# Optimization experiments

Measured on AMD Instinct MI355X. Metric: run time of the kernel, lower is better.

## Reference

```python
import jax, jax.numpy as jnp
import numpy as np
import math

# Config (matches init_kwargs): ProphetNet-style ngram self-attention
T, B, E, H, NGRAM, NB, MAXD = 512, 4, 1024, 16, 2, 32, 128
HD = E // H
TGT = (1 + NGRAM) * T
NEG = -1e9


def _buckets(rel):
    # faithful numpy version of _relative_positions_bucket (bidirectional=False)
    n = np.maximum(-rel, 0)
    max_exact = NB // 2
    is_small = n < max_exact
    large = max_exact + np.log(np.maximum(n, 1) / max_exact) / math.log(MAXD / max_exact) * (NB - max_exact)
    large = np.minimum(large, NB - 1).astype(np.int32)
    return np.where(is_small, n.astype(np.int32), large)


def setup_inputs() -> dict:
    key = jax.random.key(0)
    ks = jax.random.split(key, 4)
    s = 0.02
    # position ids 1..T (ProphetNet positions start at 1); precompute bucket tables
    pos = np.arange(1, T + 1, dtype=np.int64)[None, :].repeat(B, axis=0)          # [B,T]
    main_rel = pos[:, None, :] - pos[:, :, None]                                  # [B,T,T]
    pred_keys = np.concatenate([pos - 1, pos], axis=-1)                           # [B,2T]
    pred_rel = pred_keys[:, None, :] - pos[:, :, None]                            # [B,T,2T]
    return {
        "query": jax.random.normal(ks[0], (TGT, B, E), jnp.float32),
        "in_proj_weight": jax.random.normal(ks[1], (3 * E, E), jnp.float32) * s,
        "in_proj_bias": jnp.zeros((3 * E,), jnp.float32),
        "rel_w": jax.random.normal(ks[2], (NB * H, E), jnp.float32) * s,
        "rel_b": jnp.zeros((NB * H,), jnp.float32),
        "out_w": jax.random.normal(ks[3], (E, E), jnp.float32) * s,
        "out_b": jnp.zeros((E,), jnp.float32),
        "main_buckets": jnp.asarray(_buckets(main_rel), jnp.int32),
        "predict_buckets": jnp.asarray(_buckets(pred_rel), jnp.int32),
    }


def reference(query, in_proj_weight, in_proj_bias, rel_w, rel_b, out_w, out_b,
              main_buckets, predict_buckets):
    scaling = HD ** -0.5
    qkv = query @ in_proj_weight.T + in_proj_bias                  # [TGT,B,3E]
    q, k, v = jnp.split(qkv, 3, axis=-1)
    q = q * scaling

    def heads(x):  # [TGT,B,E] -> [B*H, TGT, HD]
        return x.reshape(TGT, B * H, HD).transpose(1, 0, 2)

    q, k, v = heads(q), heads(k), heads(v)
    q_main, k_main, v_main = q[:, :T], k[:, :T], v[:, :T]

    def ngram_split(x):  # [B*H, NGRAM*T, HD] -> [N, B*H, T, HD]
        return x[:, T:].reshape(B * H, NGRAM, T, HD).transpose(1, 0, 2, 3)

    q_pred, k_pred, v_pred = ngram_split(q), ngram_split(k), ngram_split(v)
    h_main = query[:T]                                             # [T,B,E]
    h_pred = query[T:].reshape(NGRAM, T, B, E)

    # ---------- main stream ----------
    aw_main = jnp.einsum('bth,bsh->bts', q_main, k_main)           # [B*H,T,T]
    vals = h_main.transpose(1, 0, 2) @ rel_w.T + rel_b             # [B,T,NB*H]
    vals = vals.reshape(B, T, NB, H).transpose(0, 3, 1, 2)         # [B,H,T,NB]
    idx = jnp.broadcast_to(main_buckets[:, None], (B, H, T, T))
    rel_main = jnp.take_along_axis(vals, idx, axis=-1).reshape(B * H, T, T)
    causal = jnp.triu(jnp.full((T, T), NEG, jnp.float32), 1)       # self_attn_mask
    aw_main = jax.nn.softmax(aw_main + rel_main + causal[None], axis=-1)
    attn_main = jnp.einsum('bts,bsh->bth', aw_main, v_main)        # [B*H,T,HD]
    attn_main = attn_main.transpose(1, 0, 2).reshape(1, T, B, E)
    attn_main = attn_main @ out_w.T + out_b

    # ---------- ngram predict streams ----------
    k_ng = jnp.concatenate([jnp.broadcast_to(k_main[None], (NGRAM, B * H, T, HD)), k_pred], axis=2)
    v_ng = jnp.concatenate([jnp.broadcast_to(v_main[None], (NGRAM, B * H, T, HD)), v_pred], axis=2)
    aw_ng = jnp.einsum('nbtc,nbsc->nbts', q_pred, k_ng)            # [N,B*H,T,2T]
    valsn = h_pred.transpose(0, 2, 1, 3) @ rel_w.T + rel_b         # [N,B,T,NB*H]
    valsn = valsn.reshape(NGRAM, B, T, NB, H).transpose(0, 1, 4, 2, 3)  # [N,B,H,T,NB]
    idxn = jnp.broadcast_to(predict_buckets[None, :, None], (NGRAM, B, H, T, 2 * T))
    rel_ng = jnp.take_along_axis(valsn, idxn, axis=-1).reshape(NGRAM, B * H, T, 2 * T)
    # ngram_mask: main part causal, predict part only the matching position
    ng_mask = jnp.concatenate([causal, NEG * (1.0 - jnp.eye(T, dtype=jnp.float32))], axis=1)  # [T,2T]
    aw_ng = jax.nn.softmax(aw_ng + rel_ng + ng_mask[None, None], axis=-1)
    attn_ng = jnp.einsum('nbts,nbsc->nbtc', aw_ng, v_ng)           # [N,B*H,T,HD]
    attn_ng = attn_ng.transpose(0, 2, 1, 3).reshape(NGRAM, T, B, E)
    attn_ng = attn_ng @ out_w.T + out_b

    return jnp.concatenate([attn_main, attn_ng], axis=0).reshape(TGT, B, E)
```

## Files before the change

kernel.cpp:

```cpp
#include <hip/hip_runtime.h>
#include <hip/hip_bf16.h>
#include <math.h>

constexpr int T_ = 512;
constexpr int B_ = 4;
constexpr int E_ = 1024;
constexpr int H_ = 16;
constexpr int NGRAM_ = 2;
constexpr int TGT_ = (1 + NGRAM_) * T_;
constexpr int ROWS_ = TGT_ * B_;

typedef __bf16 bf16_t;
typedef __bf16 bf16x8 __attribute__((ext_vector_type(8)));
typedef __bf16 bf16x4 __attribute__((ext_vector_type(4)));
typedef float f32x4 __attribute__((ext_vector_type(4)));

#define GLL(gaddr, laddr)                                                     \
  __builtin_amdgcn_global_load_lds(                                           \
      (const __attribute__((address_space(1))) void*)(gaddr),                 \
      (__attribute__((address_space(3))) void*)(laddr), 16, 0, 0)

#define BARX()  asm volatile("s_barrier" ::: "memory")
#define WVM7()  asm volatile("s_waitcnt vmcnt(7)" ::: "memory")
#define WVM0()  asm volatile("s_waitcnt vmcnt(0)" ::: "memory")
#define LGKM0() asm volatile("s_waitcnt lgkmcnt(0)" ::: "memory")

__global__ __launch_bounds__(256) void prep(
    const float* __restrict__ query, const float* __restrict__ ipw,
    const float* __restrict__ relw, const float* __restrict__ outw,
    bf16_t* __restrict__ qb, bf16_t* __restrict__ ipwb,
    bf16_t* __restrict__ relwb, bf16_t* __restrict__ outwb) {
  const int i = blockIdx.x * 256 + threadIdx.x;
  constexpr int N1 = ROWS_ * E_ / 4;
  constexpr int N2 = 3 * E_ * E_ / 4;
  constexpr int N3 = 512 * E_ / 4;
  constexpr int N4 = E_ * E_ / 4;
  const float4* src;
  bf16_t* dst;
  int j = i;
  if (i < N1) { src = (const float4*)query; dst = qb; }
  else if (i < N1 + N2) { src = (const float4*)ipw; dst = ipwb; j = i - N1; }
  else if (i < N1 + N2 + N3) { src = (const float4*)relw; dst = relwb; j = i - N1 - N2; }
  else if (i < N1 + N2 + N3 + N4) { src = (const float4*)outw; dst = outwb; j = i - N1 - N2 - N3; }
  else return;
  const float4 v = src[j];
  bf16x4 o;
  o[0] = (bf16_t)v.x; o[1] = (bf16_t)v.y;
  o[2] = (bf16_t)v.z; o[3] = (bf16_t)v.w;
  ((bf16x4*)dst)[j] = o;
}

__device__ __forceinline__ int sw256(int row, int col) {
  return row * 256 + ((((col >> 3) ^ (row & 31)) << 3) | (col & 7));
}

__global__ __launch_bounds__(512, 2) void bgemm_proj(
    const bf16_t* __restrict__ A, const bf16_t* __restrict__ W,
    const float* __restrict__ ipb, const float* __restrict__ relb,
    bf16_t* __restrict__ qkvb, float* __restrict__ relv2,
    bf16_t* __restrict__ vT) {
  __shared__ bf16_t smem[57344];
  bf16_t* As0 = smem;
  bf16_t* As1 = smem + 12288;
  bf16_t* Bs0 = smem + 24576;
  bf16_t* Bs1 = smem + 24576 + 16384;

  const int tid = threadIdx.x;
  const int wave = tid >> 6, lane = tid & 63;
  const int wr = wave >> 2, wc = wave & 3;
  const int pid = blockIdx.y * 14 + blockIdx.x;
  const int lid = (pid & 7) * 56 + (pid >> 3);
  const int by = lid / 14;
  const int bx = lid - by * 14;
  const int bm = by * 192, bn = bx * 256;
  const int q = lane >> 4, ln = lane & 15;
  const int grow = tid >> 3;
  const int gcol = ((tid & 7) ^ (grow & 7)) * 8;
  const int co[2] = {((q) ^ (ln & 7)) * 8, ((4 + q) ^ (ln & 7)) * 8};

  f32x4 acc[6][4];
#pragma unroll
  for (int mi = 0; mi < 6; ++mi)
#pragma unroll
    for (int ni = 0; ni < 4; ++ni)
#pragma unroll
      for (int r = 0; r < 4; ++r) acc[mi][ni][r] = 0.f;

  auto stage = [&](int kt, bf16_t* la, bf16_t* lb) {
    const int kc = kt * 64 + gcol;
#pragma unroll
    for (int p = 0; p < 3; ++p)
      GLL(&A[(size_t)(bm + p * 64 + grow) * 1024 + kc], &la[p * 4096 + tid * 8]);
#pragma unroll
    for (int p = 0; p < 4; ++p)
      GLL(&W[(size_t)(bn + p * 64 + grow) * 1024 + kc], &lb[p * 4096 + tid * 8]);
  };

  auto compute = [&](const bf16_t* la, const bf16_t* lb) {
#pragma unroll
    for (int t = 0; t < 2; ++t) {
      bf16x8 bfr[4], afr[3];
#pragma unroll
      for (int ni = 0; ni < 4; ++ni)
        bfr[ni] = *(const bf16x8*)&lb[(wc * 64 + ni * 16 + ln) * 64 + co[t]];
#pragma unroll
      for (int mi = 0; mi < 3; ++mi)
        afr[mi] = *(const bf16x8*)&la[(wr * 96 + mi * 16 + ln) * 64 + co[t]];
      BARX(); LGKM0();
      __builtin_amdgcn_s_setprio(1);
#pragma unroll
      for (int mi = 0; mi < 3; ++mi)
#pragma unroll
        for (int ni = 0; ni < 4; ++ni)
          acc[mi][ni] = __builtin_amdgcn_mfma_f32_16x16x32_bf16(
              afr[mi], bfr[ni], acc[mi][ni], 0, 0, 0);
      __builtin_amdgcn_s_setprio(0);
      BARX();
#pragma unroll
      for (int mi = 0; mi < 3; ++mi)
        afr[mi] = *(const bf16x8*)&la[(wr * 96 + (3 + mi) * 16 + ln) * 64 + co[t]];
      BARX(); LGKM0();
      __builtin_amdgcn_s_setprio(1);
#pragma unroll
      for (int mi = 0; mi < 3; ++mi)
#pragma unroll
        for (int ni = 0; ni < 4; ++ni)
          acc[3 + mi][ni] = __builtin_amdgcn_mfma_f32_16x16x32_bf16(
              afr[mi], bfr[ni], acc[3 + mi][ni], 0, 0, 0);
      __builtin_amdgcn_s_setprio(0);
      BARX();
    }
  };

  stage(0, As0, Bs0);
  stage(1, As1, Bs1);

  for (int jj = 0; jj < 8; ++jj) {
    WVM7(); BARX();
    compute(As0, Bs0);
    if (jj < 7) stage(2 * jj + 2, As0, Bs0);
    if (jj < 7) { WVM7(); } else { WVM0(); }
    BARX();
    compute(As1, Bs1);
    if (jj < 7) stage(2 * jj + 3, As1, Bs1);
  }

  if (bn < 2048) {
    const float sc = (bn < 1024) ? 0.125f : 1.0f;
#pragma unroll
    for (int mi = 0; mi < 6; ++mi) {
#pragma unroll
      for (int ni = 0; ni < 4; ++ni) {
        const int col = bn + wc * 64 + ni * 16 + ln;
        const float bv = ipb[col];
#pragma unroll
        for (int r = 0; r < 4; ++r) {
          const int row = bm + wr * 96 + mi * 16 + q * 4 + r;
          qkvb[(size_t)row * 3072 + col] = (bf16_t)((acc[mi][ni][r] + bv) * sc);
        }
      }
    }
  } else if (bn < 3072) {
    __syncthreads();
#pragma unroll
    for (int mi = 0; mi < 6; ++mi) {
#pragma unroll
      for (int ni = 0; ni < 4; ++ni) {
        const int col_l = wc * 64 + ni * 16 + ln;
        const float bv = ipb[bn + col_l];
#pragma unroll
        for (int r = 0; r < 4; ++r) {
          const int row_l = wr * 96 + mi * 16 + q * 4 + r;
          smem[sw256(row_l, col_l)] = (bf16_t)(acc[mi][ni][r] + bv);
        }
      }
    }
    __syncthreads();
    const int h0 = (bn - 2048) >> 6;
    const int tb0 = bm >> 2;
#pragma unroll
    for (int e = 0; e < 2; ++e) {
      const int task = e * 512 + tid;
      const int b = task & 3;
      const int c = task >> 2;
      const int h = h0 + (c >> 6);
      const int d = c & 63;
      const size_t base = ((size_t)((b * 16 + h) * 64 + d)) * (size_t)TGT_ + tb0;
#pragma unroll
      for (int k = 0; k < 6; ++k) {
        bf16x8 v8;
#pragma unroll
        for (int i = 0; i < 8; ++i)
          v8[i] = smem[sw256((k * 8 + i) * 4 + b, c)];
        *(bf16x8*)&vT[base + k * 8] = v8;
      }
    }
  } else {
    const int cb = bn - 3072 + wc * 64;
    float4 rb4;
#pragma unroll
    for (int ni = 0; ni < 4; ++ni)
      ((float*)&rb4)[ni] = relb[cb + ni * 16 + ln];
    const int bkbase = cb >> 4;
#pragma unroll
    for (int mi = 0; mi < 6; ++mi) {
#pragma unroll
      for (int r = 0; r < 4; ++r) {
        const int row = bm + wr * 96 + mi * 16 + q * 4 + r;
        float4 v;
        v.x = acc[mi][0][r] + rb4.x;
        v.y = acc[mi][1][r] + rb4.y;
        v.z = acc[mi][2][r] + rb4.z;
        v.w = acc[mi][3][r] + rb4.w;
        *(float4*)&relv2[(size_t)row * 512 + ln * 32 + bkbase] = v;
      }
    }
  }
}

__global__ __launch_bounds__(256, 4) void bgemm_out(
    const bf16_t* __restrict__ A, const bf16_t* __restrict__ W,
    const float* __restrict__ bias, float* __restrict__ C, int N) {
  __shared__ bf16_t As[128 * 64];
  __shared__ bf16_t Bs[128 * 64];

  const int tid = threadIdx.x;
  const int wave = tid >> 6, lane = tid & 63;
  const int wr = wave >> 1, wc = wave & 1;
  const int pid = blockIdx.y * 8 + blockIdx.x;
  const int lid = (pid & 7) * 48 + (pid >> 3);
  const int bm = (lid >> 3) * 128, bn = (lid & 7) * 128;
  const int q = lane >> 4, ln = lane & 15;
  const int grow = tid >> 3;
  const int gcol = ((tid & 7) ^ (grow & 7)) * 8;

  f32x4 acc[4][4];
#pragma unroll
  for (int mi = 0; mi < 4; ++mi)
#pragma unroll
    for (int ni = 0; ni < 4; ++ni)
#pragma unroll
      for (int r = 0; r < 4; ++r) acc[mi][ni][r] = 0.f;

  const int co[2] = {((q) ^ (ln & 7)) * 8, ((4 + q) ^ (ln & 7)) * 8};

  for (int k0 = 0; k0 < 1024; k0 += 64) {
    __syncthreads();
#pragma unroll
    for (int p = 0; p < 4; ++p) {
      GLL(&A[(size_t)(bm + p * 32 + grow) * 1024 + k0 + gcol], &As[p * 2048 + tid * 8]);
      GLL(&W[(size_t)(bn + p * 32 + grow) * 1024 + k0 + gcol], &Bs[p * 2048 + tid * 8]);
    }
    __syncthreads();
#pragma unroll
    for (int t = 0; t < 2; ++t) {
      bf16x8 af[4], bf[4];
#pragma unroll
      for (int mi = 0; mi < 4; ++mi)
        af[mi] = *(const bf16x8*)&As[(wr * 64 + mi * 16 + ln) * 64 + co[t]];
#pragma unroll
      for (int ni = 0; ni < 4; ++ni)
        bf[ni] = *(const bf16x8*)&Bs[(wc * 64 + ni * 16 + ln) * 64 + co[t]];
#pragma unroll
      for (int mi = 0; mi < 4; ++mi)
#pragma unroll
        for (int ni = 0; ni < 4; ++ni)
          acc[mi][ni] = __builtin_amdgcn_mfma_f32_16x16x32_bf16(
              af[mi], bf[ni], acc[mi][ni], 0, 0, 0);
    }
  }

#pragma unroll
  for (int mi = 0; mi < 4; ++mi) {
#pragma unroll
    for (int ni = 0; ni < 4; ++ni) {
      const int col = bn + wc * 64 + ni * 16 + ln;
      const float bv = bias[col];
#pragma unroll
      for (int r = 0; r < 4; ++r) {
        const int row = bm + wr * 64 + mi * 16 + q * 4 + r;
        C[(size_t)row * N + col] = acc[mi][ni][r] + bv;
      }
    }
  }
}

__device__ __forceinline__ int bucket_of(int n) {
  if (n < 16) return n;
  const float lf = __log2f((float)n);
  int b = (int)(16.0f + (lf - 4.0f) * 5.3333333f);
  return b > 31 ? 31 : b;
}

__global__ __launch_bounds__(256, 2) void flash_mfma(
    const bf16_t* __restrict__ qkvb, const bf16_t* __restrict__ vT,
    const float* __restrict__ relv2, bf16_t* __restrict__ attn) {
  __shared__ bf16_t Ks[2][64 * 64];
  __shared__ bf16_t Vts[2][64 * 64];
  __shared__ bf16_t Ps[4][16 * 64];
  __shared__ bf16_t biasS[3][64 * 33];

  const int qt = 7 - blockIdx.x, tq0 = qt * 64;
  const int bh = blockIdx.y, b = bh >> 4, h = bh & 15;
  const int tid = threadIdx.x;
  const int wave = tid >> 6, lane = tid & 63;
  const int q = lane >> 4, ln = lane & 15;
  const int m0 = wave * 16;
  const int grow = tid >> 3;
  const int gcol = ((tid & 7) ^ (grow & 7)) * 8;
  const int co[2] = {((q) ^ (ln & 7)) * 8, ((4 + q) ^ (ln & 7)) * 8};

#pragma unroll
  for (int z = 0; z < 3; ++z) {
#pragma unroll
    for (int u = 0; u < 2; ++u) {
      const int c = u * 256 + tid;
      const int row = c >> 3, j4 = (c & 7) * 4;
      const float4 v = *(const float4*)
          &relv2[((size_t)(z * T_ + tq0 + row) * B_ + b) * 512 + h * 32 + j4];
      biasS[z][row * 33 + j4 + 0] = (bf16_t)v.x;
      biasS[z][row * 33 + j4 + 1] = (bf16_t)v.y;
      biasS[z][row * 33 + j4 + 2] = (bf16_t)v.z;
      biasS[z][row * 33 + j4 + 3] = (bf16_t)v.w;
    }
  }

#pragma unroll
  for (int u = 0; u < 2; ++u) {
    const int sr = u * 32 + grow;
    GLL(&qkvb[((size_t)(0 * T_ + tq0 + sr) * B_ + b) * 3072 + h * 64 + gcol],
        &Ks[0][u * 2048 + tid * 8]);
    GLL(&qkvb[((size_t)(1 * T_ + tq0 + sr) * B_ + b) * 3072 + h * 64 + gcol],
        &Vts[0][u * 2048 + tid * 8]);
    GLL(&qkvb[((size_t)(2 * T_ + tq0 + sr) * B_ + b) * 3072 + h * 64 + gcol],
        &Ks[1][u * 2048 + tid * 8]);
  }
  __syncthreads();

  bf16x8 aq[3][2];
  aq[0][0] = *(const bf16x8*)&Ks[0][(m0 + ln) * 64 + co[0]];
  aq[0][1] = *(const bf16x8*)&Ks[0][(m0 + ln) * 64 + co[1]];
  aq[1][0] = *(const bf16x8*)&Vts[0][(m0 + ln) * 64 + co[0]];
  aq[1][1] = *(const bf16x8*)&Vts[0][(m0 + ln) * 64 + co[1]];
  aq[2][0] = *(const bf16x8*)&Ks[1][(m0 + ln) * 64 + co[0]];
  aq[2][1] = *(const bf16x8*)&Ks[1][(m0 + ln) * 64 + co[1]];

  float bv31[3][4], bv0[3][4];
#pragma unroll
  for (int z = 0; z < 3; ++z)
#pragma unroll
    for (int r = 0; r < 4; ++r) {
      const int rloc = m0 + q * 4 + r;
      bv31[z][r] = (float)biasS[z][rloc * 33 + 31];
      bv0[z][r] = (float)biasS[z][rloc * 33];
    }

  f32x4 Od[3][4];
  float lpart[3][4];
#pragma unroll
  for (int z = 0; z < 3; ++z)
#pragma unroll
    for (int r = 0; r < 4; ++r) {
      lpart[z][r] = 0.f;
#pragma unroll
      for (int tc = 0; tc < 4; ++tc) Od[z][tc][r] = 0.f;
    }

  const int ntiles = qt + 3;

  auto stage_tile = [&](int jj, int buf) {
    const int krb = (jj <= qt) ? jj * 64 : ((jj - qt) * T_ + tq0);
#pragma unroll
    for (int u = 0; u < 2; ++u) {
      const int sr = u * 32 + grow;
      GLL(&qkvb[((size_t)(krb + sr) * B_ + b) * 3072 + 1024 + h * 64 + gcol],
          &Ks[buf][u * 2048 + tid * 8]);
      GLL(&vT[((size_t)bh * 64 + sr) * (size_t)TGT_ + krb + gcol],
          &Vts[buf][u * 2048 + tid * 8]);
    }
  };

  __syncthreads();
  stage_tile(0, 0);
  __syncthreads();

  for (int jj = 0; jj < ntiles; ++jj) {
    const int cur = jj & 1;
    if (jj + 1 < ntiles) stage_tile(jj + 1, cur ^ 1);

    const int krb = (jj <= qt) ? jj * 64 : ((jj - qt) * T_ + tq0);

    bf16x8 kf[4][2], vf[4][2];
#pragma unroll
    for (int tc = 0; tc < 4; ++tc) {
      kf[tc][0] = *(const bf16x8*)&Ks[cur][(tc * 16 + ln) * 64 + co[0]];
      kf[tc][1] = *(const bf16x8*)&Ks[cur][(tc * 16 + ln) * 64 + co[1]];
      vf[tc][0] = *(const bf16x8*)&Vts[cur][(tc * 16 + ln) * 64 + co[0]];
      vf[tc][1] = *(const bf16x8*)&Vts[cur][(tc * 16 + ln) * 64 + co[1]];
    }

    if (jj <= qt) {
      const bool far = (jj <= qt - 3);
#pragma unroll
      for (int z = 0; z < 3; ++z) {
        f32x4 acc[4];
#pragma unroll
        for (int tc = 0; tc < 4; ++tc)
#pragma unroll
          for (int r = 0; r < 4; ++r) acc[tc][r] = 0.f;
#pragma unroll
        for (int tc = 0; tc < 4; ++tc) {
          acc[tc] = __builtin_amdgcn_mfma_f32_16x16x32_bf16(aq[z][0], kf[tc][0], acc[tc], 0, 0, 0);
          acc[tc] = __builtin_amdgcn_mfma_f32_16x16x32_bf16(aq[z][1], kf[tc][1], acc[tc], 0, 0, 0);
        }

        if (far) {
#pragma unroll
          for (int r = 0; r < 4; ++r) {
            const float bv = bv31[z][r];
#pragma unroll
            for (int tc = 0; tc < 4; ++tc) {
              const float p = __expf(acc[tc][r] + bv);
              lpart[z][r] += p;
              const int pc = (tc * 2 + (ln >> 3)) ^ ((q * 4 + r) & 7);
              Ps[wave][(q * 4 + r) * 64 + pc * 8 + (ln & 7)] = (bf16_t)p;
            }
          }
        } else {
#pragma unroll
          for (int r = 0; r < 4; ++r) {
            const int rloc = m0 + q * 4 + r;
            const int dbase = tq0 + rloc - krb;
#pragma unroll
            for (int tc = 0; tc < 4; ++tc) {
              const int sl = tc * 16 + ln;
              const int d = dbase - sl;
              const bool valid = (jj < qt) | (d >= 0);
              int n = d < 0 ? 0 : d;
              if (z > 0) n += 1;
              const float bv = (float)biasS[z][rloc * 33 + bucket_of(n)];
              const float p = valid ? __expf(acc[tc][r] + bv) : 0.f;
              lpart[z][r] += p;
              const int pc = (tc * 2 + (ln >> 3)) ^ ((q * 4 + r) & 7);
              Ps[wave][(q * 4 + r) * 64 + pc * 8 + (ln & 7)] = (bf16_t)p;
            }
          }
        }

        bf16x8 ap[2];
        ap[0] = *(const bf16x8*)&Ps[wave][ln * 64 + co[0]];
        ap[1] = *(const bf16x8*)&Ps[wave][ln * 64 + co[1]];
#pragma unroll
        for (int tc = 0; tc < 4; ++tc) {
          Od[z][tc] = __builtin_amdgcn_mfma_f32_16x16x32_bf16(ap[0], vf[tc][0], Od[z][tc], 0, 0, 0);
          Od[z][tc] = __builtin_amdgcn_mfma_f32_16x16x32_bf16(ap[1], vf[tc][1], Od[z][tc], 0, 0, 0);
        }
      }
    } else {
#pragma unroll
      for (int z = 1; z <= 2; ++z) {
        if (jj - qt == z) {
          f32x4 acc[4];
#pragma unroll
          for (int tc = 0; tc < 4; ++tc)
#pragma unroll
            for (int r = 0; r < 4; ++r) acc[tc][r] = 0.f;
#pragma unroll
          for (int tc = 0; tc < 4; ++tc) {
            acc[tc] = __builtin_amdgcn_mfma_f32_16x16x32_bf16(aq[z][0], kf[tc][0], acc[tc], 0, 0, 0);
            acc[tc] = __builtin_amdgcn_mfma_f32_16x16x32_bf16(aq[z][1], kf[tc][1], acc[tc], 0, 0, 0);
          }
#pragma unroll
          for (int r = 0; r < 4; ++r) {
            const int rloc = m0 + q * 4 + r;
            const float bv = bv0[z][r];
#pragma unroll
            for (int tc = 0; tc < 4; ++tc) {
              const int sl = tc * 16 + ln;
              const float p = (sl == rloc) ? __expf(acc[tc][r] + bv) : 0.f;
              lpart[z][r] += p;
              const int pc = (tc * 2 + (ln >> 3)) ^ ((q * 4 + r) & 7);
              Ps[wave][(q * 4 + r) * 64 + pc * 8 + (ln & 7)] = (bf16_t)p;
            }
          }
          bf16x8 ap[2];
          ap[0] = *(const bf16x8*)&Ps[wave][ln * 64 + co[0]];
          ap[1] = *(const bf16x8*)&Ps[wave][ln * 64 + co[1]];
#pragma unroll
          for (int tc = 0; tc < 4; ++tc) {
            Od[z][tc] = __builtin_amdgcn_mfma_f32_16x16x32_bf16(ap[0], vf[tc][0], Od[z][tc], 0, 0, 0);
            Od[z][tc] = __builtin_amdgcn_mfma_f32_16x16x32_bf16(ap[1], vf[tc][1], Od[z][tc], 0, 0, 0);
          }
        }
      }
    }
    __syncthreads();
  }

#pragma unroll
  for (int z = 0; z < 3; ++z) {
#pragma unroll
    for (int r = 0; r < 4; ++r) {
      float l = lpart[z][r];
      l += __shfl_xor(l, 1, 16);
      l += __shfl_xor(l, 2, 16);
      l += __shfl_xor(l, 4, 16);
      l += __shfl_xor(l, 8, 16);
      const float inv = 1.f / l;
      const size_t rowbase =
          ((size_t)(z * T_ + tq0 + m0 + q * 4 + r) * B_ + b) * (size_t)E_ + h * 64;
#pragma unroll
      for (int tc = 0; tc < 4; ++tc)
        attn[rowbase + tc * 16 + ln] = (bf16_t)(Od[z][tc][r] * inv);
    }
  }
}

extern "C" void kernel_launch(void* const* d_in, const int* in_sizes, int n_in,
                              void* d_out, int out_size, void* d_ws, size_t ws_size,
                              hipStream_t stream) {
  const float* query = (const float*)d_in[0];
  const float* ipw   = (const float*)d_in[1];
  const float* ipb   = (const float*)d_in[2];
  const float* relw  = (const float*)d_in[3];
  const float* relb  = (const float*)d_in[4];
  const float* outw  = (const float*)d_in[5];
  const float* outb  = (const float*)d_in[6];
  float* out = (float*)d_out;

  bf16_t* qkvb  = (bf16_t*)d_ws;
  float*  relv2 = (float*)(qkvb + (size_t)ROWS_ * 3 * E_);
  bf16_t* qb    = (bf16_t*)(relv2 + (size_t)ROWS_ * 512);
  bf16_t* ipwb  = qb + (size_t)ROWS_ * E_;
  bf16_t* relwb = ipwb + (size_t)(3 * E_) * E_;
  bf16_t* outwb = relwb + (size_t)512 * E_;
  bf16_t* attnb = outwb + (size_t)E_ * E_;
  bf16_t* vT    = attnb + (size_t)ROWS_ * E_;

  const dim3 blk(256);

  {
    const int ntot = (ROWS_ * E_ + 3 * E_ * E_ + 512 * E_ + E_ * E_) / 4;
    prep<<<dim3((ntot + 255) / 256), blk, 0, stream>>>(
        query, ipw, relw, outw, qb, ipwb, relwb, outwb);
  }

  bgemm_proj<<<dim3(3584 / 256, ROWS_ / 192), dim3(512), 0, stream>>>(
      qb, ipwb, ipb, relb, qkvb, relv2, vT);

  flash_mfma<<<dim3(8, B_ * H_), blk, 0, stream>>>(
      qkvb, vT, relv2, attnb);

  bgemm_out<<<dim3(E_ / 128, ROWS_ / 128), blk, 0, stream>>>(
      attnb, outwb, outb, out, E_);
}
```

Measured before the change: 240.6 us.

## Enlarge projection GEMM tile to 256x256 with interleaved sub-tile prefetch

```diff
diff --git a/kernel.cpp b/kernel.cpp
--- a/kernel.cpp
+++ b/kernel.cpp
@@ -21,7 +21,8 @@
       (__attribute__((address_space(3))) void*)(laddr), 16, 0, 0)
 
 #define BARX()  asm volatile("s_barrier" ::: "memory")
-#define WVM7()  asm volatile("s_waitcnt vmcnt(7)" ::: "memory")
+#define WVM8()  asm volatile("s_waitcnt vmcnt(8)" ::: "memory")
+#define WVM4()  asm volatile("s_waitcnt vmcnt(4)" ::: "memory")
 #define WVM0()  asm volatile("s_waitcnt vmcnt(0)" ::: "memory")
 #define LGKM0() asm volatile("s_waitcnt lgkmcnt(0)" ::: "memory")
 
@@ -59,103 +60,133 @@
     const float* __restrict__ ipb, const float* __restrict__ relb,
     bf16_t* __restrict__ qkvb, float* __restrict__ relv2,
     bf16_t* __restrict__ vT) {
-  __shared__ bf16_t smem[57344];
-  bf16_t* As0 = smem;
-  bf16_t* As1 = smem + 12288;
-  bf16_t* Bs0 = smem + 24576;
-  bf16_t* Bs1 = smem + 24576 + 16384;
+  __shared__ __align__(16) bf16_t smem[65536];
 
   const int tid = threadIdx.x;
   const int wave = tid >> 6, lane = tid & 63;
   const int wr = wave >> 2, wc = wave & 3;
   const int pid = blockIdx.y * 14 + blockIdx.x;
-  const int lid = (pid & 7) * 56 + (pid >> 3);
+  const int lid = (pid & 7) * 42 + (pid >> 3);
   const int by = lid / 14;
   const int bx = lid - by * 14;
-  const int bm = by * 192, bn = bx * 256;
+  const int bm = by * 256, bn = bx * 256;
   const int q = lane >> 4, ln = lane & 15;
   const int grow = tid >> 3;
   const int gcol = ((tid & 7) ^ (grow & 7)) * 8;
   const int co[2] = {((q) ^ (ln & 7)) * 8, ((4 + q) ^ (ln & 7)) * 8};
 
-  f32x4 acc[6][4];
-#pragma unroll
-  for (int mi = 0; mi < 6; ++mi)
+  f32x4 acc[8][4];
+#pragma unroll
+  for (int mi = 0; mi < 8; ++mi)
 #pragma unroll
     for (int ni = 0; ni < 4; ++ni)
 #pragma unroll
       for (int r = 0; r < 4; ++r) acc[mi][ni][r] = 0.f;
 
-  auto stage = [&](int kt, bf16_t* la, bf16_t* lb) {
-    const int kc = kt * 64 + gcol;
-#pragma unroll
-    for (int p = 0; p < 3; ++p)
-      GLL(&A[(size_t)(bm + p * 64 + grow) * 1024 + kc], &la[p * 4096 + tid * 8]);
-#pragma unroll
-    for (int p = 0; p < 4; ++p)
-      GLL(&W[(size_t)(bn + p * 64 + grow) * 1024 + kc], &lb[p * 4096 + tid * 8]);
+  auto stA = [&](int kt, int row0) {
+    bf16_t* dst = smem + (kt & 1) * 32768 + row0 * 64;
+    GLL(&A[(size_t)(bm + row0 + grow) * 1024 + kt * 64 + gcol], &dst[tid * 8]);
   };
-
-  auto compute = [&](const bf16_t* la, const bf16_t* lb) {
-#pragma unroll
-    for (int t = 0; t < 2; ++t) {
-      bf16x8 bfr[4], afr[3];
+  auto stB = [&](int kt, int row0) {
+    bf16_t* dst = smem + (kt & 1) * 32768 + 16384 + row0 * 64;
+    GLL(&W[(size_t)(bn + row0 + grow) * 1024 + kt * 64 + gcol], &dst[tid * 8]);
+  };
+
+  stA(0, 0); stA(0, 128); stB(0, 0); stB(0, 64);
+  stB(0, 128); stB(0, 192); stA(0, 64); stA(0, 192);
+  stA(1, 0); stA(1, 128); stB(1, 0); stB(1, 64);
+  stB(1, 128); stB(1, 192); stA(1, 64); stA(1, 192);
+  WVM8();
+  BARX();
+
+#pragma unroll 1
+  for (int kt = 0; kt < 16; ++kt) {
+    const bf16_t* As = smem + (kt & 1) * 32768;
+    const bf16_t* Bs = As + 16384;
+    if (kt) {
+      if (kt == 15) { WVM0(); } else { WVM4(); }
+      BARX();
+    }
+    bf16x8 b0[4], b1[4], a[4];
+
+#pragma unroll
+    for (int ni = 0; ni < 4; ++ni)
+      b0[ni] = *(const bf16x8*)&Bs[(wc * 64 + ni * 16 + ln) * 64 + co[0]];
+#pragma unroll
+    for (int mi = 0; mi < 4; ++mi)
+      a[mi] = *(const bf16x8*)&As[(wr * 128 + mi * 16 + ln) * 64 + co[0]];
+    if (kt >= 1 && kt <= 14) { stB(kt + 1, 128); stB(kt + 1, 192); }
+    BARX(); LGKM0();
+    __builtin_amdgcn_s_setprio(1);
+#pragma unroll
+    for (int mi = 0; mi < 4; ++mi)
 #pragma unroll
       for (int ni = 0; ni < 4; ++ni)
-        bfr[ni] = *(const bf16x8*)&lb[(wc * 64 + ni * 16 + ln) * 64 + co[t]];
-#pragma unroll
-      for (int mi = 0; mi < 3; ++mi)
-        afr[mi] = *(const bf16x8*)&la[(wr * 96 + mi * 16 + ln) * 64 + co[t]];
-      BARX(); LGKM0();
-      __builtin_amdgcn_s_setprio(1);
-#pragma unroll
-      for (int mi = 0; mi < 3; ++mi)
-#pragma unroll
-        for (int ni = 0; ni < 4; ++ni)
-          acc[mi][ni] = __builtin_amdgcn_mfma_f32_16x16x32_bf16(
-              afr[mi], bfr[ni], acc[mi][ni], 0, 0, 0);
-      __builtin_amdgcn_s_setprio(0);
-      BARX();
-#pragma unroll
-      for (int mi = 0; mi < 3; ++mi)
-        afr[mi] = *(const bf16x8*)&la[(wr * 96 + (3 + mi) * 16 + ln) * 64 + co[t]];
-      BARX(); LGKM0();
-      __builtin_amdgcn_s_setprio(1);
-#pragma unroll
-      for (int mi = 0; mi < 3; ++mi)
-#pragma unroll
-        for (int ni = 0; ni < 4; ++ni)
-          acc[3 + mi][ni] = __builtin_amdgcn_mfma_f32_16x16x32_bf16(
-              afr[mi], bfr[ni], acc[3 + mi][ni], 0, 0, 0);
-      __builtin_amdgcn_s_setprio(0);
-      BARX();
-    }
-  };
-
-  stage(0, As0, Bs0);
-  stage(1, As1, Bs1);
-
-  for (int jj = 0; jj < 8; ++jj) {
-    WVM7(); BARX();
-    compute(As0, Bs0);
-    if (jj < 7) stage(2 * jj + 2, As0, Bs0);
-    if (jj < 7) { WVM7(); } else { WVM0(); }
+        acc[mi][ni] = __builtin_amdgcn_mfma_f32_16x16x32_bf16(
+            a[mi], b0[ni], acc[mi][ni], 0, 0, 0);
+    __builtin_amdgcn_s_setprio(0);
     BARX();
-    compute(As1, Bs1);
-    if (jj < 7) stage(2 * jj + 3, As1, Bs1);
+
+#pragma unroll
+    for (int ni = 0; ni < 4; ++ni)
+      b1[ni] = *(const bf16x8*)&Bs[(wc * 64 + ni * 16 + ln) * 64 + co[1]];
+#pragma unroll
+    for (int mi = 0; mi < 4; ++mi)
+      a[mi] = *(const bf16x8*)&As[(wr * 128 + mi * 16 + ln) * 64 + co[1]];
+    if (kt >= 1 && kt <= 14) { stA(kt + 1, 64); stA(kt + 1, 192); }
+    BARX(); LGKM0();
+    __builtin_amdgcn_s_setprio(1);
+#pragma unroll
+    for (int mi = 0; mi < 4; ++mi)
+#pragma unroll
+      for (int ni = 0; ni < 4; ++ni)
+        acc[mi][ni] = __builtin_amdgcn_mfma_f32_16x16x32_bf16(
+            a[mi], b1[ni], acc[mi][ni], 0, 0, 0);
+    __builtin_amdgcn_s_setprio(0);
+    BARX();
+
+#pragma unroll
+    for (int mi = 0; mi < 4; ++mi)
+      a[mi] = *(const bf16x8*)&As[(wr * 128 + 64 + mi * 16 + ln) * 64 + co[0]];
+    if (kt <= 13) { stA(kt + 2, 0); stA(kt + 2, 128); }
+    BARX(); LGKM0();
+    __builtin_amdgcn_s_setprio(1);
+#pragma unroll
+    for (int mi = 0; mi < 4; ++mi)
+#pragma unroll
+      for (int ni = 0; ni < 4; ++ni)
+        acc[4 + mi][ni] = __builtin_amdgcn_mfma_f32_16x16x32_bf16(
+            a[mi], b0[ni], acc[4 + mi][ni], 0, 0, 0);
+    __builtin_amdgcn_s_setprio(0);
+    BARX();
+
+#pragma unroll
+    for (int mi = 0; mi < 4; ++mi)
+      a[mi] = *(const bf16x8*)&As[(wr * 128 + 64 + mi * 16 + ln) * 64 + co[1]];
+    if (kt <= 13) { stB(kt + 2, 0); stB(kt + 2, 64); }
+    BARX(); LGKM0();
+    __builtin_amdgcn_s_setprio(1);
+#pragma unroll
+    for (int mi = 0; mi < 4; ++mi)
+#pragma unroll
+      for (int ni = 0; ni < 4; ++ni)
+        acc[4 + mi][ni] = __builtin_amdgcn_mfma_f32_16x16x32_bf16(
+            a[mi], b1[ni], acc[4 + mi][ni], 0, 0, 0);
+    __builtin_amdgcn_s_setprio(0);
+    BARX();
   }
 
   if (bn < 2048) {
     const float sc = (bn < 1024) ? 0.125f : 1.0f;
 #pragma unroll
-    for (int mi = 0; mi < 6; ++mi) {
+    for (int mi = 0; mi < 8; ++mi) {
 #pragma unroll
       for (int ni = 0; ni < 4; ++ni) {
         const int col = bn + wc * 64 + ni * 16 + ln;
         const float bv = ipb[col];
 #pragma unroll
         for (int r = 0; r < 4; ++r) {
-          const int row = bm + wr * 96 + mi * 16 + q * 4 + r;
+          const int row = bm + wr * 128 + mi * 16 + q * 4 + r;
           qkvb[(size_t)row * 3072 + col] = (bf16_t)((acc[mi][ni][r] + bv) * sc);
         }
       }
@@ -163,14 +194,14 @@
   } else if (bn < 3072) {
     __syncthreads();
 #pragma unroll
-    for (int mi = 0; mi < 6; ++mi) {
+    for (int mi = 0; mi < 8; ++mi) {
 #pragma unroll
       for (int ni = 0; ni < 4; ++ni) {
         const int col_l = wc * 64 + ni * 16 + ln;
         const float bv = ipb[bn + col_l];
 #pragma unroll
         for (int r = 0; r < 4; ++r) {
-          const int row_l = wr * 96 + mi * 16 + q * 4 + r;
+          const int row_l = wr * 128 + mi * 16 + q * 4 + r;
           smem[sw256(row_l, col_l)] = (bf16_t)(acc[mi][ni][r] + bv);
         }
       }
@@ -187,7 +218,7 @@
       const int d = c & 63;
       const size_t base = ((size_t)((b * 16 + h) * 64 + d)) * (size_t)TGT_ + tb0;
 #pragma unroll
-      for (int k = 0; k < 6; ++k) {
+      for (int k = 0; k < 8; ++k) {
         bf16x8 v8;
 #pragma unroll
         for (int i = 0; i < 8; ++i)
@@ -203,10 +234,10 @@
       ((float*)&rb4)[ni] = relb[cb + ni * 16 + ln];
     const int bkbase = cb >> 4;
 #pragma unroll
-    for (int mi = 0; mi < 6; ++mi) {
+    for (int mi = 0; mi < 8; ++mi) {
 #pragma unroll
       for (int r = 0; r < 4; ++r) {
-        const int row = bm + wr * 96 + mi * 16 + q * 4 + r;
+        const int row = bm + wr * 128 + mi * 16 + q * 4 + r;
         float4 v;
         v.x = acc[mi][0][r] + rb4.x;
         v.y = acc[mi][1][r] + rb4.y;
@@ -545,7 +576,7 @@
         query, ipw, relw, outw, qb, ipwb, relwb, outwb);
   }
 
-  bgemm_proj<<<dim3(3584 / 256, ROWS_ / 192), dim3(512), 0, stream>>>(
+  bgemm_proj<<<dim3(3584 / 256, ROWS_ / 256), dim3(512), 0, stream>>>(
       qb, ipwb, ipb, relb, qkvb, relv2, vT);
 
   flash_mfma<<<dim3(8, B_ * H_), blk, 0, stream>>>(
```

Measured after the change: 257.2 us. 1.07x slower.
